# Performance work log

Hardware: AMD Instinct MI355X
Metric: run time of the kernel (lower is better)

## Reference

```python
import jax, jax.numpy as jnp
import numpy as np

D_MODEL = 96
D_STATE = 16
D_INNER = 192   # expand * d_model
DT_RANK = 6     # ceil(96/16)
D_DEPTH_OUT = 1024  # (64/2)*(64/2)
BATCH, HH, WW = 2, 64, 64


def silu(v):
    return v * jax.nn.sigmoid(v)


def setup_inputs() -> dict:
    key = jax.random.key(0)
    ks = jax.random.split(key, 10)
    f = jnp.float32
    x = jax.random.normal(ks[0], (BATCH, HH, WW, D_MODEL), f)
    in_proj_w = jax.random.normal(ks[1], (2 * D_INNER, D_MODEL), f) * 0.02
    conv2d_w = jax.random.normal(ks[2], (D_INNER, 1, 3, 3), f) * 0.1  # depthwise, groups=D_INNER
    conv2d_b = jnp.zeros((D_INNER,), f)
    depth_conv_w = jax.random.normal(ks[3], (D_INNER, 1, 3, 3), f) * 0.1  # depthwise, stride 2
    depth_conv_b = jnp.zeros((D_INNER,), f)
    depth_fc_w = jax.random.normal(ks[4], (D_INNER, D_DEPTH_OUT), f) * 0.02
    depth_fc_b = jnp.zeros((D_INNER,), f)
    x_proj_w = jax.random.normal(ks[5], (DT_RANK + 2 * D_STATE, D_INNER), f) * 0.02
    dt_init_std = DT_RANK ** (-0.5)
    dt_projs_w = jax.random.uniform(ks[6], (D_INNER, DT_RANK), f, -dt_init_std, dt_init_std)
    # inverse-softplus of dt ~ U(log 1e-3, log 0.1)
    dt = jnp.exp(jax.random.uniform(ks[7], (D_INNER,), f) * (np.log(0.1) - np.log(0.001)) + np.log(0.001))
    dt = jnp.clip(dt, 1e-4, None)
    dt_projs_b = dt + jnp.log(-jnp.expm1(-dt))
    A_logs = jnp.log(jnp.tile(jnp.arange(1, D_STATE + 1, dtype=f)[None, :], (D_INNER, 1)))
    Ds = jnp.ones((D_INNER,), f)
    out_norm_w = jnp.ones((D_INNER,), f)
    out_norm_b = jnp.zeros((D_INNER,), f)
    out_proj_w = jax.random.normal(ks[8], (D_MODEL, D_INNER), f) * 0.02
    return dict(x=x, in_proj_w=in_proj_w, conv2d_w=conv2d_w, conv2d_b=conv2d_b,
                depth_conv_w=depth_conv_w, depth_conv_b=depth_conv_b,
                depth_fc_w=depth_fc_w, depth_fc_b=depth_fc_b, x_proj_w=x_proj_w,
                dt_projs_w=dt_projs_w, dt_projs_b=dt_projs_b, A_logs=A_logs, Ds=Ds,
                out_norm_w=out_norm_w, out_norm_b=out_norm_b, out_proj_w=out_proj_w)


def _selective_scan(u, delta, A, Bm, Cm, D, delta_bias):
    # u, delta: [B, D, L]; A: [D, N]; Bm, Cm: [B, N, L]; D: [D]; delta_bias: [D]
    delta = jax.nn.softplus(delta + delta_bias[None, :, None])
    dA = jnp.exp(jnp.einsum('bdl,dn->lbdn', delta, A))          # [L,B,D,N]
    dBu = jnp.einsum('bdl,bnl,bdl->lbdn', delta, Bm, u)          # [L,B,D,N]
    Ct = jnp.transpose(Cm, (2, 0, 1))                            # [L,B,N]
    h0 = jnp.zeros(dA.shape[1:], u.dtype)

    def step(h, inp):
        a, b, c = inp
        h = a * h + b                                            # S6 recurrence
        return h, jnp.einsum('bdn,bn->bd', h, c)

    _, ys = jax.lax.scan(step, h0, (dA, dBu, Ct))                # ys: [L,B,D]
    y = jnp.transpose(ys, (1, 2, 0))                             # [B,D,L]
    return y + D[None, :, None] * u


def _forward(x, in_proj_w, conv2d_w, conv2d_b, depth_conv_w, depth_conv_b,
             depth_fc_w, depth_fc_b, x_proj_w, dt_projs_w, dt_projs_b,
             A_logs, Ds, out_norm_w, out_norm_b, out_proj_w):
    B, H, W, _ = x.shape
    Di, N, R = D_INNER, D_STATE, DT_RANK
    dn = ('NCHW', 'OIHW', 'NCHW')
    xz = x @ in_proj_w.T
    x1, z = jnp.split(xz, 2, axis=-1)
    xc = jnp.transpose(x1, (0, 3, 1, 2))                         # [B,Di,H,W]
    xc = jax.lax.conv_general_dilated(xc, conv2d_w, (1, 1), [(1, 1), (1, 1)],
                                      dimension_numbers=dn, feature_group_count=Di)
    xc = silu(xc + conv2d_b[None, :, None, None])
    dxc = jax.lax.conv_general_dilated(xc, depth_conv_w, (2, 2), [(1, 1), (1, 1)],
                                       dimension_numbers=dn, feature_group_count=Di)
    dxc = dxc + depth_conv_b[None, :, None, None]                # [B,Di,H/2,W/2]
    dx = dxc.reshape(B, Di, -1)                                  # [B,Di,1024]
    dx = dx @ depth_fc_w.T + depth_fc_b                          # [B,Di,Di]
    dx = silu(jnp.transpose(dx, (0, 2, 1)))                      # [B,Di,CC], CC=Di
    L = H * W
    CC = dx.shape[-1]
    xs = jnp.concatenate([dx, xc.reshape(B, Di, L)], axis=-1)    # mode='head': [B,Di,LL]
    x_dbl = jnp.einsum('bdl,cd->bcl', xs, x_proj_w)
    dts, Bm, Cm = x_dbl[:, :R], x_dbl[:, R:R + N], x_dbl[:, R + N:]
    dts = jnp.einsum('brl,dr->bdl', dts, dt_projs_w)
    A = -jnp.exp(A_logs)
    y = _selective_scan(xs, dts, A, Bm, Cm, Ds, dt_projs_b)
    y = y[..., CC:]                                              # drop depth tokens (head mode)
    y = jnp.transpose(y, (0, 2, 1)).reshape(B, H, W, Di)
    mu = jnp.mean(y, axis=-1, keepdims=True)
    var = jnp.var(y, axis=-1, keepdims=True)
    y = (y - mu) * jax.lax.rsqrt(var + 1e-5) * out_norm_w + out_norm_b
    y = y * silu(z)
    return y @ out_proj_w.T


def reference(x, in_proj_w, conv2d_w, conv2d_b, depth_conv_w, depth_conv_b,
              depth_fc_w, depth_fc_b, x_proj_w, dt_projs_w, dt_projs_b,
              A_logs, Ds, out_norm_w, out_norm_b, out_proj_w):
    return _forward(x, in_proj_w, conv2d_w, conv2d_b, depth_conv_w, depth_conv_b,
                    depth_fc_w, depth_fc_b, x_proj_w, dt_projs_w, dt_projs_b,
                    A_logs, Ds, out_norm_w, out_norm_b, out_proj_w)
```

## Files before the change

kernel.cpp:

```cpp
#include <hip/hip_runtime.h>
#include <hip/hip_bf16.h>

typedef __hip_bfloat16 bf16;

#define BATCH 2
#define DM 96
#define DI 192
#define LSP 4096
#define LD 192
#define LTOT 4288
#define NST 16
#define RK 6
#define DFC 1024
#define CLEN 64
#define NCH 67
#define XR 16

__device__ __forceinline__ float b2f(bf16 v) { return __bfloat162float(v); }
__device__ __forceinline__ float silu_f(float x) { return x / (1.f + __expf(-x)); }
__device__ __forceinline__ float softplus_f(float x) { return x > 20.f ? x : log1pf(__expf(x)); }

__device__ __forceinline__ int is_f32(const void* alog) {
    return ((const unsigned int*)alog)[0] == 0u;
}
__device__ __forceinline__ float LDI(const void* p, int i, int f32m) {
    return f32m ? ((const float*)p)[i] : __bfloat162float(((const bf16*)p)[i]);
}
__device__ __forceinline__ void unpack2(unsigned int u, float* o) {
    o[0] = __uint_as_float(u << 16);
    o[1] = __uint_as_float(u & 0xffff0000u);
}

__global__ __launch_bounds__(768) void k_inproj(const void* __restrict__ x, const void* __restrict__ ipw,
                                                const void* __restrict__ alog,
                                                float* __restrict__ x1, float* __restrict__ z) {
    __shared__ uint4 sxr[384];
    const int f32m = is_f32(alog);
    int t = threadIdx.x;
    int col = t >> 1;
    int kh = t & 1;
    int row0 = blockIdx.x * 16;
    float wr[48];
    if (f32m) {
        const float4* wp = (const float4*)((const float*)ipw + col * 96 + kh * 48);
        #pragma unroll
        for (int i = 0; i < 12; i++) {
            float4 v = wp[i];
            wr[4*i] = v.x; wr[4*i+1] = v.y; wr[4*i+2] = v.z; wr[4*i+3] = v.w;
        }
        if (t < 384) sxr[t] = ((const uint4*)((const float*)x + row0 * 96))[t];
        __syncthreads();
        for (int r = 0; r < 16; r++) {
            const uint4* xr = &sxr[r * 24 + kh * 12];
            float acc = 0.f;
            #pragma unroll
            for (int i = 0; i < 12; i++) {
                uint4 u = xr[i];
                acc += __uint_as_float(u.x) * wr[4*i]   + __uint_as_float(u.y) * wr[4*i+1]
                     + __uint_as_float(u.z) * wr[4*i+2] + __uint_as_float(u.w) * wr[4*i+3];
            }
            acc += __shfl_xor(acc, 1);
            if (kh == 0) {
                int row = row0 + r;
                if (col < DI) x1[row * DI + col] = acc;
                else          z[row * DI + (col - DI)] = acc;
            }
        }
    } else {
        const uint4* wp = (const uint4*)((const bf16*)ipw + col * 96 + kh * 48);
        #pragma unroll
        for (int i = 0; i < 6; i++) {
            uint4 v = wp[i];
            unpack2(v.x, &wr[8*i]);   unpack2(v.y, &wr[8*i+2]);
            unpack2(v.z, &wr[8*i+4]); unpack2(v.w, &wr[8*i+6]);
        }
        if (t < 192) sxr[t] = ((const uint4*)((const bf16*)x + row0 * 96))[t];
        __syncthreads();
        for (int r = 0; r < 16; r++) {
            const uint4* xr = &sxr[r * 12 + kh * 6];
            float acc = 0.f;
            #pragma unroll
            for (int i = 0; i < 6; i++) {
                uint4 xv = xr[i];
                float xf8[8];
                unpack2(xv.x, &xf8[0]); unpack2(xv.y, &xf8[2]);
                unpack2(xv.z, &xf8[4]); unpack2(xv.w, &xf8[6]);
                #pragma unroll
                for (int j = 0; j < 8; j++) acc += xf8[j] * wr[8*i + j];
            }
            acc += __shfl_xor(acc, 1);
            if (kh == 0) {
                int row = row0 + r;
                if (col < DI) x1[row * DI + col] = acc;
                else          z[row * DI + (col - DI)] = acc;
            }
        }
    }
}

__global__ __launch_bounds__(192) void k_conv1(const float* __restrict__ x1, const void* __restrict__ cw,
                                               const void* __restrict__ cb, float* __restrict__ xs,
                                               const void* __restrict__ alog) {
    const int f32m = is_f32(alog);
    int d = threadIdx.x;
    int blk = blockIdx.x;
    int b = blk >> 12, l = blk & 4095;
    int h = l >> 6, w_ = l & 63;
    float acc = LDI(cb, d, f32m);
    #pragma unroll
    for (int dh = 0; dh < 3; dh++) {
        int hh = h + dh - 1;
        if ((unsigned)hh >= 64u) continue;
        #pragma unroll
        for (int dw = 0; dw < 3; dw++) {
            int ww = w_ + dw - 1;
            if ((unsigned)ww >= 64u) continue;
            acc += x1[((b << 12) + (hh << 6) + ww) * DI + d] * LDI(cw, d * 9 + dh * 3 + dw, f32m);
        }
    }
    xs[(b * LTOT + LD + l) * DI + d] = silu_f(acc);
}

__global__ __launch_bounds__(192) void k_conv2(const float* __restrict__ xs, const void* __restrict__ dw,
                                               const void* __restrict__ db, float* __restrict__ dxc,
                                               const void* __restrict__ alog) {
    const int f32m = is_f32(alog);
    int d = threadIdx.x;
    int blk = blockIdx.x;
    int b = blk >> 10, lp = blk & 1023;
    int hp = lp >> 5, wp = lp & 31;
    float acc = LDI(db, d, f32m);
    #pragma unroll
    for (int dh = 0; dh < 3; dh++) {
        int h = 2 * hp + dh - 1;
        if ((unsigned)h >= 64u) continue;
        #pragma unroll
        for (int dw_ = 0; dw_ < 3; dw_++) {
            int w_ = 2 * wp + dw_ - 1;
            if ((unsigned)w_ >= 64u) continue;
            acc += xs[(b * LTOT + LD + (h << 6) + w_) * DI + d] * LDI(dw, d * 9 + dh * 3 + dw_, f32m);
        }
    }
    dxc[(b * DFC + lp) * DI + d] = acc;
}

__global__ __launch_bounds__(192) void k_dfc(const float* __restrict__ dxc, const void* __restrict__ fw,
                                             float* __restrict__ part, const void* __restrict__ alog) {
    __shared__ float sfw[4 * 256];
    const int f32m = is_f32(alog);
    int t = threadIdx.x;
    int blk = blockIdx.x;
    int p = blk / 96;
    int rem = blk - p * 96;
    int b   = rem / 48;
    int ch0 = (rem % 48) * 4;
    int k0  = p * 256;
    for (int idx = t; idx < 4 * 256; idx += 192)
        sfw[idx] = LDI(fw, (ch0 + (idx >> 8)) * DFC + k0 + (idx & 255), f32m);
    __syncthreads();
    float a0 = 0.f, a1 = 0.f, a2 = 0.f, a3 = 0.f;
    #pragma unroll 8
    for (int k = 0; k < 256; k++) {
        float dv = dxc[(b * DFC + k0 + k) * DI + t];
        a0 += dv * sfw[k];
        a1 += dv * sfw[256 + k];
        a2 += dv * sfw[512 + k];
        a3 += dv * sfw[768 + k];
    }
    int ob = ((p * 2 + b) * 192 + t) * DI + ch0;
    *(float4*)&part[ob] = make_float4(a0, a1, a2, a3);
}

__global__ __launch_bounds__(256) void k_xdbl(const float* __restrict__ xs_r, float* __restrict__ xs_w,
                                              const float* __restrict__ part, const void* __restrict__ fb,
                                              const void* __restrict__ xpw,
                                              const void* __restrict__ dtw, const void* __restrict__ dtb,
                                              float* __restrict__ BCb, float* __restrict__ del,
                                              const void* __restrict__ alog) {
    __shared__ float sw[38 * 193];
    __shared__ float srow[XR][193];
    __shared__ float sdtw[DI * RK];
    __shared__ float sdtb[DI];
    __shared__ float sxd6[XR][8];
    const int f32m = is_f32(alog);
    int t = threadIdx.x;
    for (int c = t >> 3; c < 38; c += 32) {
        int seg = (t & 7) * 24;
        for (int k = seg; k < seg + 24; k++) sw[c * 193 + k] = LDI(xpw, c * DI + k, f32m);
    }
    for (int idx = t; idx < DI * RK; idx += 256) sdtw[idx] = LDI(dtw, idx, f32m);
    if (t < DI) sdtb[t] = LDI(dtb, t, f32m);
    int row0 = blockIdx.x * XR;
    int bb = row0 >= LTOT ? 1 : 0;
    int depth = (row0 - bb * LTOT) < LD;
    for (int idx = t; idx < XR * DI; idx += 256) {
        int row = idx / DI, k = idx - row * DI;
        int grow = row0 + row;
        float v;
        if (depth) {
            int tok = grow - bb * LTOT;
            int o = (bb * 192 + tok) * DI + k;
            v = part[o] + part[o + 73728] + part[o + 147456] + part[o + 221184];
            v = silu_f(v + LDI(fb, k, f32m));
            xs_w[grow * DI + k] = v;
        } else {
            v = xs_r[grow * DI + k];
        }
        srow[row][k] = v;
    }
    __syncthreads();
    int r = t & 15, cg = t >> 4;
    float a0 = 0.f, a1 = 0.f, a2 = 0.f;
    const float* w0 = &sw[cg * 193];
    const float* w1 = &sw[(cg + 16) * 193];
    const float* w2 = (cg < 6) ? &sw[(cg + 32) * 193] : &sw[cg * 193];
    const float* xr = srow[r];
    #pragma unroll 8
    for (int k = 0; k < DI; k++) {
        float xv = xr[k];
        a0 += xv * w0[k];
        a1 += xv * w1[k];
        a2 += xv * w2[k];
    }
    int grow = row0 + r;
    if (cg < 6) sxd6[r][cg] = a0;
    else        BCb[grow * 32 + (cg - 6)] = a0;
    BCb[grow * 32 + (cg + 10)] = a1;
    if (cg < 6) BCb[grow * 32 + (cg + 26)] = a2;
    __syncthreads();
    float xd0 = sxd6[r][0], xd1 = sxd6[r][1], xd2 = sxd6[r][2];
    float xd3 = sxd6[r][3], xd4 = sxd6[r][4], xd5 = sxd6[r][5];
    #pragma unroll
    for (int dd = 0; dd < 12; dd++) {
        int d = cg * 12 + dd;
        const float* wv = &sdtw[d * RK];
        float dtv = sdtb[d] + xd0 * wv[0] + xd1 * wv[1] + xd2 * wv[2]
                            + xd3 * wv[3] + xd4 * wv[4] + xd5 * wv[5];
        srow[r][d] = softplus_f(dtv);
    }
    __syncthreads();
    for (int idx = t; idx < XR * DI; idx += 256) {
        int row = idx / DI, k = idx - row * DI;
        del[(row0 + row) * DI + k] = srow[row][k];
    }
}

__global__ __launch_bounds__(256) void k_scan1(const float* __restrict__ del, const float* __restrict__ xs,
                                               const float* __restrict__ BCb, const void* __restrict__ alog,
                                               float* __restrict__ Af, float* __restrict__ hf) {
    __shared__ float sdel[CLEN * 16];
    __shared__ float su[CLEN * 16];
    __shared__ float sbc[CLEN * 32];
    const int f32m = is_f32(alog);
    int t = threadIdx.x;
    int beta = blockIdx.x;
    int b = beta / (12 * NCH);
    int rem = beta - b * (12 * NCH);
    int dblk = rem / NCH, ch = rem - dblk * NCH;
    int d0 = dblk * 16, l0 = ch * CLEN;
    int bL = b * LTOT;
    for (int idx = t; idx < CLEN * 16; idx += 256) {
        int i = idx >> 4, dd = idx & 15;
        sdel[idx] = del[(bL + l0 + i) * DI + d0 + dd];
        su[idx]   = xs [(bL + l0 + i) * DI + d0 + dd];
    }
    for (int idx = t; idx < CLEN * 32; idx += 256) {
        int i = idx >> 5, c = idx & 31;
        sbc[idx] = BCb[(bL + l0 + i) * 32 + c];
    }
    __syncthreads();
    int dloc = t >> 4, n = t & 15;
    int d = d0 + dloc;
    float A = -__expf(LDI(alog, d * NST + n, f32m));
    float h = 0.f, ap = 1.f;
    #pragma unroll 4
    for (int i = 0; i < CLEN; i++) {
        float dt = sdel[(i << 4) | dloc];
        float u  = su[(i << 4) | dloc];
        float Bv = sbc[(i << 5) | n];
        float a = __expf(dt * A);
        h = a * h + dt * Bv * u;
        ap *= a;
    }
    int o = ((b * DI + d) * NCH + ch) * NST + n;
    Af[o] = ap;
    hf[o] = h;
}

__global__ __launch_bounds__(256) void k_scan2(const float* __restrict__ Af, const float* __restrict__ hf,
                                               float* __restrict__ He) {
    int t = threadIdx.x;
    int g = blockIdx.x * 16 + (t >> 4);
    int n = t & 15;
    int base = g * NCH * NST + n;
    float h = 0.f;
    for (int ch = 0; ch < NCH; ch++) {
        int o = base + ch * NST;
        He[o] = h;
        h = Af[o] * h + hf[o];
    }
}

__global__ __launch_bounds__(256) void k_scan3(const float* __restrict__ del, const float* __restrict__ xs,
                                               const float* __restrict__ BCb, const void* __restrict__ alog,
                                               const void* __restrict__ Dsv, const float* __restrict__ He,
                                               float* __restrict__ y) {
    __shared__ float sdel[CLEN * 16];
    __shared__ float su[CLEN * 16];
    __shared__ float sbc[CLEN * 32];
    const int f32m = is_f32(alog);
    int t = threadIdx.x;
    int beta = blockIdx.x;
    int b = beta / (12 * NCH);
    int rem = beta - b * (12 * NCH);
    int dblk = rem / NCH, ch = rem - dblk * NCH;
    int d0 = dblk * 16, l0 = ch * CLEN;
    int bL = b * LTOT;
    for (int idx = t; idx < CLEN * 16; idx += 256) {
        int i = idx >> 4, dd = idx & 15;
        sdel[idx] = del[(bL + l0 + i) * DI + d0 + dd];
        su[idx]   = xs [(bL + l0 + i) * DI + d0 + dd];
    }
    for (int idx = t; idx < CLEN * 32; idx += 256) {
        int i = idx >> 5, c = idx & 31;
        sbc[idx] = BCb[(bL + l0 + i) * 32 + c];
    }
    __syncthreads();
    int dloc = t >> 4, n = t & 15;
    int d = d0 + dloc;
    float A = -__expf(LDI(alog, d * NST + n, f32m));
    float Dv = LDI(Dsv, d, f32m);
    float h = He[((b * DI + d) * NCH + ch) * NST + n];
    for (int i = 0; i < CLEN; i++) {
        float dt = sdel[(i << 4) | dloc];
        float u  = su[(i << 4) | dloc];
        float Bv = sbc[(i << 5) | n];
        float Cv = sbc[(i << 5) | 16 | n];
        float a = __expf(dt * A);
        h = a * h + dt * Bv * u;
        float yv = h * Cv;
        #pragma unroll
        for (int m = 8; m; m >>= 1) yv += __shfl_xor(yv, m, 16);
        int l = l0 + i;
        if (n == 0 && l >= LD) y[(b * LSP + (l - LD)) * DI + d] = yv + Dv * u;
    }
}

__global__ __launch_bounds__(384) void k_out(const float* __restrict__ y, const float* __restrict__ z,
                                             const void* __restrict__ nw, const void* __restrict__ nb,
                                             const void* __restrict__ opw, void* __restrict__ out,
                                             const void* __restrict__ alog) {
    __shared__ float sg[2][DI];
    __shared__ float sred[2][2][3];
    const int f32m = is_f32(alog);
    int t = threadIdx.x;
    int m = t >> 2, kh = t & 3;
    float wr[48];
    if (f32m) {
        const float4* wp = (const float4*)((const float*)opw + m * DI + kh * 48);
        #pragma unroll
        for (int i = 0; i < 12; i++) {
            float4 v = wp[i];
            wr[4*i] = v.x; wr[4*i+1] = v.y; wr[4*i+2] = v.z; wr[4*i+3] = v.w;
        }
    } else {
        const uint4* wp = (const uint4*)((const bf16*)opw + m * DI + kh * 48);
        #pragma unroll
        for (int i = 0; i < 6; i++) {
            uint4 v = wp[i];
            unpack2(v.x, &wr[8*i]);   unpack2(v.y, &wr[8*i+2]);
            unpack2(v.z, &wr[8*i+4]); unpack2(v.w, &wr[8*i+6]);
        }
    }
    float nwv = 0.f, nbv = 0.f;
    if (t < DI) { nwv = LDI(nw, t, f32m); nbv = LDI(nb, t, f32m); }
    int wv_ = t >> 6;
    int row0 = blockIdx.x * 16;
    for (int pr = 0; pr < 8; pr++) {
        int r0 = row0 + pr * 2, r1 = r0 + 1;
        float y0 = 0.f, z0 = 0.f, y1 = 0.f, z1 = 0.f;
        if (t < DI) {
            y0 = y[r0 * DI + t]; z0 = z[r0 * DI + t];
            y1 = y[r1 * DI + t]; z1 = z[r1 * DI + t];
            float s0 = y0, q0 = y0 * y0, s1 = y1, q1 = y1 * y1;
            #pragma unroll
            for (int off = 32; off; off >>= 1) {
                s0 += __shfl_xor(s0, off); q0 += __shfl_xor(q0, off);
                s1 += __shfl_xor(s1, off); q1 += __shfl_xor(q1, off);
            }
            if ((t & 63) == 0) {
                sred[0][0][wv_] = s0; sred[0][1][wv_] = q0;
                sred[1][0][wv_] = s1; sred[1][1][wv_] = q1;
            }
        }
        __syncthreads();
        if (t < DI) {
            float S0  = sred[0][0][0] + sred[0][0][1] + sred[0][0][2];
            float Q0  = sred[0][1][0] + sred[0][1][1] + sred[0][1][2];
            float S1  = sred[1][0][0] + sred[1][0][1] + sred[1][0][2];
            float Q1  = sred[1][1][0] + sred[1][1][1] + sred[1][1][2];
            float mu0 = S0 * (1.f / 192.f), var0 = Q0 * (1.f / 192.f) - mu0 * mu0;
            float mu1 = S1 * (1.f / 192.f), var1 = Q1 * (1.f / 192.f) - mu1 * mu1;
            float g0 = (y0 - mu0) * rsqrtf(var0 + 1e-5f) * nwv + nbv;
            g0 *= z0 / (1.f + __expf(-z0));
            float g1 = (y1 - mu1) * rsqrtf(var1 + 1e-5f) * nwv + nbv;
            g1 *= z1 / (1.f + __expf(-z1));
            sg[0][t] = g0;
            sg[1][t] = g1;
        }
        __syncthreads();
        const float* g0p = &sg[0][kh * 48];
        const float* g1p = &sg[1][kh * 48];
        float a0 = 0.f, a1 = 0.f;
        #pragma unroll
        for (int j = 0; j < 48; j++) {
            a0 += g0p[j] * wr[j];
            a1 += g1p[j] * wr[j];
        }
        a0 += __shfl_xor(a0, 1); a0 += __shfl_xor(a0, 2);
        a1 += __shfl_xor(a1, 1); a1 += __shfl_xor(a1, 2);
        if (kh == 0) {
            if (f32m) {
                ((float*)out)[r0 * DM + m] = a0;
                ((float*)out)[r1 * DM + m] = a1;
            } else {
                ((bf16*)out)[r0 * DM + m] = __float2bfloat16(a0);
                ((bf16*)out)[r1 * DM + m] = __float2bfloat16(a1);
            }
        }
    }
}

extern "C" void kernel_launch(void* const* d_in, const int* in_sizes, int n_in,
                              void* d_out, int out_size, void* d_ws, size_t ws_size,
                              hipStream_t stream) {
    (void)in_sizes; (void)n_in; (void)out_size; (void)ws_size;
    const void* x    = d_in[0];
    const void* ipw  = d_in[1];
    const void* c1w  = d_in[2];
    const void* c1b  = d_in[3];
    const void* c2w  = d_in[4];
    const void* c2b  = d_in[5];
    const void* fcw  = d_in[6];
    const void* fcb  = d_in[7];
    const void* xpw  = d_in[8];
    const void* dtw  = d_in[9];
    const void* dtb  = d_in[10];
    const void* alog = d_in[11];
    const void* Dsv  = d_in[12];
    const void* nw   = d_in[13];
    const void* nb   = d_in[14];
    const void* opw  = d_in[15];

    float* ws  = (float*)d_ws;
    float* x1  = ws;
    float* z   = x1  + BATCH * LSP * DI;
    float* xs  = z   + BATCH * LSP * DI;
    float* dxc = xs  + BATCH * LTOT * DI;
    float* BCb = dxc + BATCH * DFC * DI;
    float* del = BCb + BATCH * LTOT * 32;
    float* Af  = del + BATCH * LTOT * DI;
    float* hf  = Af  + BATCH * DI * NCH * NST;
    float* He  = hf  + BATCH * DI * NCH * NST;
    float* part = x1;
    float* y    = x1;

    k_inproj<<<dim3(512), dim3(768), 0, stream>>>(x, ipw, alog, x1, z);
    k_conv1 <<<dim3(BATCH * LSP), dim3(DI), 0, stream>>>(x1, c1w, c1b, xs, alog);
    k_conv2 <<<dim3(BATCH * DFC), dim3(DI), 0, stream>>>(xs, c2w, c2b, dxc, alog);
    k_dfc   <<<dim3(384), dim3(DI), 0, stream>>>(dxc, fcw, part, alog);
    k_xdbl  <<<dim3(536), dim3(256), 0, stream>>>(xs, xs, part, fcb, xpw, dtw, dtb, BCb, del, alog);
    k_scan1 <<<dim3(BATCH * 12 * NCH), dim3(256), 0, stream>>>(del, xs, BCb, alog, Af, hf);
    k_scan2 <<<dim3(24), dim3(256), 0, stream>>>(Af, hf, He);
    k_scan3 <<<dim3(BATCH * 12 * NCH), dim3(256), 0, stream>>>(del, xs, BCb, alog, Dsv, He, y);
    k_out   <<<dim3(512), dim3(384), 0, stream>>>(y, z, nw, nb, opw, d_out, alog);
}
```

Baseline: 251.2 us.

## Recompute delta inside scan kernels, drop scan2, split dfc K, vectorize x_proj

```diff
diff --git a/kernel.cpp b/kernel.cpp
--- a/kernel.cpp
+++ b/kernel.cpp
@@ -146,7 +146,7 @@
 
 __global__ __launch_bounds__(192) void k_dfc(const float* __restrict__ dxc, const void* __restrict__ fw,
                                              float* __restrict__ part, const void* __restrict__ alog) {
-    __shared__ float sfw[4 * 256];
+    __shared__ float sfw[4 * 128];
     const int f32m = is_f32(alog);
     int t = threadIdx.x;
     int blk = blockIdx.x;
@@ -154,18 +154,18 @@
     int rem = blk - p * 96;
     int b   = rem / 48;
     int ch0 = (rem % 48) * 4;
-    int k0  = p * 256;
-    for (int idx = t; idx < 4 * 256; idx += 192)
-        sfw[idx] = LDI(fw, (ch0 + (idx >> 8)) * DFC + k0 + (idx & 255), f32m);
+    int k0  = p * 128;
+    for (int idx = t; idx < 4 * 128; idx += 192)
+        sfw[idx] = LDI(fw, (ch0 + (idx >> 7)) * DFC + k0 + (idx & 127), f32m);
     __syncthreads();
     float a0 = 0.f, a1 = 0.f, a2 = 0.f, a3 = 0.f;
     #pragma unroll 8
-    for (int k = 0; k < 256; k++) {
+    for (int k = 0; k < 128; k++) {
         float dv = dxc[(b * DFC + k0 + k) * DI + t];
         a0 += dv * sfw[k];
-        a1 += dv * sfw[256 + k];
-        a2 += dv * sfw[512 + k];
-        a3 += dv * sfw[768 + k];
+        a1 += dv * sfw[128 + k];
+        a2 += dv * sfw[256 + k];
+        a3 += dv * sfw[384 + k];
     }
     int ob = ((p * 2 + b) * 192 + t) * DI + ch0;
     *(float4*)&part[ob] = make_float4(a0, a1, a2, a3);
@@ -174,22 +174,16 @@
 __global__ __launch_bounds__(256) void k_xdbl(const float* __restrict__ xs_r, float* __restrict__ xs_w,
                                               const float* __restrict__ part, const void* __restrict__ fb,
                                               const void* __restrict__ xpw,
-                                              const void* __restrict__ dtw, const void* __restrict__ dtb,
-                                              float* __restrict__ BCb, float* __restrict__ del,
+                                              float* __restrict__ BCb, float* __restrict__ dts,
                                               const void* __restrict__ alog) {
-    __shared__ float sw[38 * 193];
-    __shared__ float srow[XR][193];
-    __shared__ float sdtw[DI * RK];
-    __shared__ float sdtb[DI];
-    __shared__ float sxd6[XR][8];
+    __shared__ float sw[38 * 196];
+    __shared__ float srow[XR][196];
     const int f32m = is_f32(alog);
     int t = threadIdx.x;
     for (int c = t >> 3; c < 38; c += 32) {
         int seg = (t & 7) * 24;
-        for (int k = seg; k < seg + 24; k++) sw[c * 193 + k] = LDI(xpw, c * DI + k, f32m);
-    }
-    for (int idx = t; idx < DI * RK; idx += 256) sdtw[idx] = LDI(dtw, idx, f32m);
-    if (t < DI) sdtb[t] = LDI(dtb, t, f32m);
+        for (int k = seg; k < seg + 24; k++) sw[c * 196 + k] = LDI(xpw, c * DI + k, f32m);
+    }
     int row0 = blockIdx.x * XR;
     int bb = row0 >= LTOT ? 1 : 0;
     int depth = (row0 - bb * LTOT) < LD;
@@ -200,7 +194,9 @@
         if (depth) {
             int tok = grow - bb * LTOT;
             int o = (bb * 192 + tok) * DI + k;
-            v = part[o] + part[o + 73728] + part[o + 147456] + part[o + 221184];
+            v = 0.f;
+            #pragma unroll
+            for (int p = 0; p < 8; p++) v += part[o + p * 73728];
             v = silu_f(v + LDI(fb, k, f32m));
             xs_w[grow * DI + k] = v;
         } else {
@@ -211,46 +207,69 @@
     __syncthreads();
     int r = t & 15, cg = t >> 4;
     float a0 = 0.f, a1 = 0.f, a2 = 0.f;
-    const float* w0 = &sw[cg * 193];
-    const float* w1 = &sw[(cg + 16) * 193];
-    const float* w2 = (cg < 6) ? &sw[(cg + 32) * 193] : &sw[cg * 193];
-    const float* xr = srow[r];
-    #pragma unroll 8
-    for (int k = 0; k < DI; k++) {
-        float xv = xr[k];
-        a0 += xv * w0[k];
-        a1 += xv * w1[k];
-        a2 += xv * w2[k];
+    const float4* w0 = (const float4*)&sw[cg * 196];
+    const float4* w1 = (const float4*)&sw[(cg + 16) * 196];
+    const float4* w2 = (const float4*)&sw[(cg < 6 ? cg + 32 : cg) * 196];
+    const float4* xr = (const float4*)&srow[r][0];
+    #pragma unroll 4
+    for (int k = 0; k < 48; k++) {
+        float4 xv = xr[k], v0 = w0[k], v1 = w1[k], v2 = w2[k];
+        a0 += xv.x * v0.x + xv.y * v0.y + xv.z * v0.z + xv.w * v0.w;
+        a1 += xv.x * v1.x + xv.y * v1.y + xv.z * v1.z + xv.w * v1.w;
+        a2 += xv.x * v2.x + xv.y * v2.y + xv.z * v2.z + xv.w * v2.w;
     }
     int grow = row0 + r;
-    if (cg < 6) sxd6[r][cg] = a0;
+    if (cg < 6) dts[grow * 6 + cg] = a0;
     else        BCb[grow * 32 + (cg - 6)] = a0;
     BCb[grow * 32 + (cg + 10)] = a1;
     if (cg < 6) BCb[grow * 32 + (cg + 26)] = a2;
+}
+
+__device__ __forceinline__ void scan_stage(const float* __restrict__ dts, const float* __restrict__ xs,
+                                           const float* __restrict__ BCb, const void* __restrict__ dtw,
+                                           const void* __restrict__ dtb, int f32m,
+                                           int bL, int l0, int d0, int t,
+                                           float* su, float* sbc, float* sdel,
+                                           float* sdts, float* sdwb) {
+    {
+        int e = t * 4;
+        int i = e >> 4, dd = e & 15;
+        *(float4*)&su[e] = *(const float4*)&xs[(bL + l0 + i) * DI + d0 + dd];
+    }
+    #pragma unroll
+    for (int q = 0; q < 2; q++) {
+        int e = (t + q * 256) * 4;
+        int i = e >> 5, c = e & 31;
+        *(float4*)&sbc[e] = *(const float4*)&BCb[(bL + l0 + i) * 32 + c];
+    }
+    for (int idx = t; idx < CLEN * RK; idx += 256) sdts[idx] = dts[(bL + l0) * RK + idx];
+    if (t < 96)            sdwb[t] = LDI(dtw, (d0 + t / 6) * RK + (t % 6), f32m);
+    else if (t < 112)      sdwb[t] = LDI(dtb, d0 + (t - 96), f32m);
     __syncthreads();
-    float xd0 = sxd6[r][0], xd1 = sxd6[r][1], xd2 = sxd6[r][2];
-    float xd3 = sxd6[r][3], xd4 = sxd6[r][4], xd5 = sxd6[r][5];
-    #pragma unroll
-    for (int dd = 0; dd < 12; dd++) {
-        int d = cg * 12 + dd;
-        const float* wv = &sdtw[d * RK];
-        float dtv = sdtb[d] + xd0 * wv[0] + xd1 * wv[1] + xd2 * wv[2]
-                            + xd3 * wv[3] + xd4 * wv[4] + xd5 * wv[5];
-        srow[r][d] = softplus_f(dtv);
+    {
+        int e = t * 4;
+        int i = e >> 4, dl = e & 15;
+        #pragma unroll
+        for (int q = 0; q < 4; q++) {
+            int dlq = dl + q;
+            float dv = sdwb[96 + dlq];
+            #pragma unroll
+            for (int r2 = 0; r2 < RK; r2++) dv += sdts[i * RK + r2] * sdwb[dlq * RK + r2];
+            sdel[e + q] = softplus_f(dv);
+        }
     }
     __syncthreads();
-    for (int idx = t; idx < XR * DI; idx += 256) {
-        int row = idx / DI, k = idx - row * DI;
-        del[(row0 + row) * DI + k] = srow[row][k];
-    }
-}
-
-__global__ __launch_bounds__(256) void k_scan1(const float* __restrict__ del, const float* __restrict__ xs,
-                                               const float* __restrict__ BCb, const void* __restrict__ alog,
+}
+
+__global__ __launch_bounds__(256) void k_scan1(const float* __restrict__ dts, const float* __restrict__ xs,
+                                               const float* __restrict__ BCb, const void* __restrict__ dtw,
+                                               const void* __restrict__ dtb, const void* __restrict__ alog,
                                                float* __restrict__ Af, float* __restrict__ hf) {
-    __shared__ float sdel[CLEN * 16];
     __shared__ float su[CLEN * 16];
     __shared__ float sbc[CLEN * 32];
+    __shared__ float sdel[CLEN * 16];
+    __shared__ float sdts[CLEN * RK];
+    __shared__ float sdwb[112];
     const int f32m = is_f32(alog);
     int t = threadIdx.x;
     int beta = blockIdx.x;
@@ -259,16 +278,7 @@
     int dblk = rem / NCH, ch = rem - dblk * NCH;
     int d0 = dblk * 16, l0 = ch * CLEN;
     int bL = b * LTOT;
-    for (int idx = t; idx < CLEN * 16; idx += 256) {
-        int i = idx >> 4, dd = idx & 15;
-        sdel[idx] = del[(bL + l0 + i) * DI + d0 + dd];
-        su[idx]   = xs [(bL + l0 + i) * DI + d0 + dd];
-    }
-    for (int idx = t; idx < CLEN * 32; idx += 256) {
-        int i = idx >> 5, c = idx & 31;
-        sbc[idx] = BCb[(bL + l0 + i) * 32 + c];
-    }
-    __syncthreads();
+    scan_stage(dts, xs, BCb, dtw, dtb, f32m, bL, l0, d0, t, su, sbc, sdel, sdts, sdwb);
     int dloc = t >> 4, n = t & 15;
     int d = d0 + dloc;
     float A = -__expf(LDI(alog, d * NST + n, f32m));
@@ -287,27 +297,17 @@
     hf[o] = h;
 }
 
-__global__ __launch_bounds__(256) void k_scan2(const float* __restrict__ Af, const float* __restrict__ hf,
-                                               float* __restrict__ He) {
-    int t = threadIdx.x;
-    int g = blockIdx.x * 16 + (t >> 4);
-    int n = t & 15;
-    int base = g * NCH * NST + n;
-    float h = 0.f;
-    for (int ch = 0; ch < NCH; ch++) {
-        int o = base + ch * NST;
-        He[o] = h;
-        h = Af[o] * h + hf[o];
-    }
-}
-
-__global__ __launch_bounds__(256) void k_scan3(const float* __restrict__ del, const float* __restrict__ xs,
-                                               const float* __restrict__ BCb, const void* __restrict__ alog,
-                                               const void* __restrict__ Dsv, const float* __restrict__ He,
+__global__ __launch_bounds__(256) void k_scan3(const float* __restrict__ dts, const float* __restrict__ xs,
+                                               const float* __restrict__ BCb, const void* __restrict__ dtw,
+                                               const void* __restrict__ dtb, const void* __restrict__ alog,
+                                               const void* __restrict__ Dsv,
+                                               const float* __restrict__ Af, const float* __restrict__ hf,
                                                float* __restrict__ y) {
-    __shared__ float sdel[CLEN * 16];
     __shared__ float su[CLEN * 16];
     __shared__ float sbc[CLEN * 32];
+    __shared__ float sdel[CLEN * 16];
+    __shared__ float sdts[CLEN * RK];
+    __shared__ float sdwb[112];
     const int f32m = is_f32(alog);
     int t = threadIdx.x;
     int beta = blockIdx.x;
@@ -316,21 +316,17 @@
     int dblk = rem / NCH, ch = rem - dblk * NCH;
     int d0 = dblk * 16, l0 = ch * CLEN;
     int bL = b * LTOT;
-    for (int idx = t; idx < CLEN * 16; idx += 256) {
-        int i = idx >> 4, dd = idx & 15;
-        sdel[idx] = del[(bL + l0 + i) * DI + d0 + dd];
-        su[idx]   = xs [(bL + l0 + i) * DI + d0 + dd];
-    }
-    for (int idx = t; idx < CLEN * 32; idx += 256) {
-        int i = idx >> 5, c = idx & 31;
-        sbc[idx] = BCb[(bL + l0 + i) * 32 + c];
-    }
-    __syncthreads();
+    scan_stage(dts, xs, BCb, dtw, dtb, f32m, bL, l0, d0, t, su, sbc, sdel, sdts, sdwb);
     int dloc = t >> 4, n = t & 15;
     int d = d0 + dloc;
     float A = -__expf(LDI(alog, d * NST + n, f32m));
     float Dv = LDI(Dsv, d, f32m);
-    float h = He[((b * DI + d) * NCH + ch) * NST + n];
+    int base = ((b * DI + d) * NCH) * NST + n;
+    float h = 0.f;
+    for (int c = 0; c < ch; c++) {
+        int oo = base + c * NST;
+        h = Af[oo] * h + hf[oo];
+    }
     for (int i = 0; i < CLEN; i++) {
         float dt = sdel[(i << 4) | dloc];
         float u  = su[(i << 4) | dloc];
@@ -458,20 +454,18 @@
     float* xs  = z   + BATCH * LSP * DI;
     float* dxc = xs  + BATCH * LTOT * DI;
     float* BCb = dxc + BATCH * DFC * DI;
-    float* del = BCb + BATCH * LTOT * 32;
-    float* Af  = del + BATCH * LTOT * DI;
+    float* dts = BCb + BATCH * LTOT * 32;
+    float* Af  = dts + BATCH * LTOT * RK;
     float* hf  = Af  + BATCH * DI * NCH * NST;
-    float* He  = hf  + BATCH * DI * NCH * NST;
     float* part = x1;
     float* y    = x1;
 
     k_inproj<<<dim3(512), dim3(768), 0, stream>>>(x, ipw, alog, x1, z);
     k_conv1 <<<dim3(BATCH * LSP), dim3(DI), 0, stream>>>(x1, c1w, c1b, xs, alog);
     k_conv2 <<<dim3(BATCH * DFC), dim3(DI), 0, stream>>>(xs, c2w, c2b, dxc, alog);
-    k_dfc   <<<dim3(384), dim3(DI), 0, stream>>>(dxc, fcw, part, alog);
-    k_xdbl  <<<dim3(536), dim3(256), 0, stream>>>(xs, xs, part, fcb, xpw, dtw, dtb, BCb, del, alog);
-    k_scan1 <<<dim3(BATCH * 12 * NCH), dim3(256), 0, stream>>>(del, xs, BCb, alog, Af, hf);
-    k_scan2 <<<dim3(24), dim3(256), 0, stream>>>(Af, hf, He);
-    k_scan3 <<<dim3(BATCH * 12 * NCH), dim3(256), 0, stream>>>(del, xs, BCb, alog, Dsv, He, y);
+    k_dfc   <<<dim3(768), dim3(DI), 0, stream>>>(dxc, fcw, part, alog);
+    k_xdbl  <<<dim3(536), dim3(256), 0, stream>>>(xs, xs, part, fcb, xpw, BCb, dts, alog);
+    k_scan1 <<<dim3(BATCH * 12 * NCH), dim3(256), 0, stream>>>(dts, xs, BCb, dtw, dtb, alog, Af, hf);
+    k_scan3 <<<dim3(BATCH * 12 * NCH), dim3(256), 0, stream>>>(dts, xs, BCb, dtw, dtb, alog, Dsv, Af, hf, y);
     k_out   <<<dim3(512), dim3(384), 0, stream>>>(y, z, nw, nb, opw, d_out, alog);
 }
```

After: 236.1 us. 6.0% less time.
